# Optimization experiments

Measured on AMD Instinct MI355X. Metric: run time of the kernel, lower is better.

Reference implementation:

```python
import math
import jax, jax.numpy as jnp
import numpy as np

N = 2048          # batch size
D = 256           # embedding_dim
MEM = 16384       # memory_size
ANOMALY_WEIGHT = 1.0
TEMP = 0.1
MOMENTUM = 0.01
NCLS = 2          # binary phishing labels -> max(labels.max()+1, 2) == 2


def setup_inputs() -> dict:
    key = jax.random.key(0)
    ks = jax.random.split(key, 10)
    s = 1.0 / math.sqrt(D)  # nn.Linear default init range
    return {
        'z': jax.random.normal(ks[0], (N, D), jnp.float32),
        'labels': jax.random.randint(ks[1], (N,), 0, NCLS),
        'memory': jax.random.normal(ks[2], (MEM, D), jnp.float32),
        'memory_weights': jax.random.uniform(ks[3], (MEM,), jnp.float32),
        'running_mean': jnp.zeros((D,), jnp.float32),
        'running_cov': jnp.eye(D, dtype=jnp.float32),
        'Wq': jax.random.uniform(ks[4], (D, D), jnp.float32, -s, s),
        'bq': jax.random.uniform(ks[5], (D,), jnp.float32, -s, s),
        'Wk': jax.random.uniform(ks[6], (D, D), jnp.float32, -s, s),
        'bk': jax.random.uniform(ks[7], (D,), jnp.float32, -s, s),
        'Wv': jax.random.uniform(ks[8], (D, D), jnp.float32, -s, s),
        'bv': jax.random.uniform(ks[9], (D,), jnp.float32, -s, s),
    }


def reference(z, labels, memory, memory_weights, running_mean, running_cov,
              Wq, bq, Wk, bk, Wv, bv):
    # ---- update(z.detach(), labels): entire update path is detached in torch ----
    z_sg = jax.lax.stop_gradient(z)

    # _update_stats: EMA of batch mean / covariance (done before importance)
    mu = z_sg.mean(axis=0)                                  # [D]
    zc = z_sg - mu
    cov = zc.T @ zc / max(N - 1, 1)                         # [D, D]
    rm = (1.0 - MOMENTUM) * running_mean + MOMENTUM * mu
    rc = (1.0 - MOMENTUM) * running_cov + MOMENTUM * cov

    # _mahalanobis with updated running stats
    c = z_sg - rm
    cov_inv = jnp.linalg.inv(rc + 1e-6 * jnp.eye(D, dtype=rc.dtype))
    dist = jnp.sqrt(jnp.clip(jnp.einsum('nd,de,ne->n', c, cov_inv, c), 1e-8))
    a_norm = (dist - dist.min()) / (dist.max() - dist.min() + 1e-8)

    # _mi_proxy: KL(batch label dist || uniform), broadcast to all items
    counts = jnp.zeros((NCLS,), z.dtype).at[labels].add(1.0)
    p = counts / jnp.clip(counts.sum(), 1.0)
    # p / uniform == p * NCLS; clip inside log for safety (both classes present)
    kl = jnp.clip((p * jnp.log(jnp.clip(p * NCLS, 1e-8))).sum(), 0.0)
    importance = (1.0 + ANOMALY_WEIGHT * a_norm) * kl       # [N]

    # serial top-1 priority-queue eviction, in descending-importance order
    order = jnp.argsort(-importance)
    z_ord = z_sg[order]
    imp_ord = importance[order]

    def evict_step(state, inp):
        mem, w = state
        zi, imp = inp
        j = jnp.argmin(w)                   # weakest memory slot
        rep = imp > w[j]
        mem = mem.at[j].set(jnp.where(rep, zi, mem[j]))
        w = w.at[j].set(jnp.where(rep, imp, w[j]))
        return (mem, w), None

    (mem, _), _ = jax.lax.scan(evict_step, (memory, memory_weights), (z_ord, imp_ord))

    # ---- query(z): cross-attention over the (full) updated memory ----
    Q = z @ Wq.T + bq                       # [N, D]
    K = mem @ Wk.T + bk                     # [MEM, D]
    V = mem @ Wv.T + bv                     # [MEM, D]
    sc = (Q @ K.T) / math.sqrt(D)           # [N, MEM]
    attn = jax.nn.softmax(sc / TEMP, axis=-1)
    return z + 0.5 * (attn @ V)
```

## Files before the change

kernel.cpp:

```cpp
#include <hip/hip_runtime.h>
#include <math.h>

#define NB   2048
#define DE   256
#define MEMN 16384
#define CAND_CAP 256
#define FSPL 16
#define FKPS 1024
#define FIT  32

typedef __attribute__((ext_vector_type(8)))  short  short8;
typedef __attribute__((ext_vector_type(16))) float  float16;

static const size_t OFF_QB   = 0;
static const size_t OFF_KB   = 262144;
static const size_t OFF_VTB  = 2359296;
static const size_t OFF_LP   = 4456448;
static const size_t OFF_OPB  = 4521984;
static const size_t SO_A    = 0;
static const size_t SO_X    = 65536;
static const size_t SO_MUP  = 131072;
static const size_t SO_DIST = 147456;

__device__ inline unsigned short f2bf(float f) {
  unsigned u = __float_as_uint(f);
  unsigned r = (u + 0x7fffu + ((u >> 16) & 1u)) >> 16;
  return (unsigned short)r;
}
__device__ inline float bf2f(unsigned short s) {
  return __uint_as_float((unsigned)s << 16);
}

__device__ inline void bitonic_sort_u64(unsigned long long* key, int n, int tid, int nth) {
  for (int k = 2; k <= n; k <<= 1) {
    for (int j = k >> 1; j > 0; j >>= 1) {
      __syncthreads();
      for (int i = tid; i < n; i += nth) {
        int ixj = i ^ j;
        if (ixj > i) {
          unsigned long long a = key[i], b = key[ixj];
          bool up = ((i & k) == 0);
          if ((a > b) == up) { key[i] = b; key[ixj] = a; }
        }
      }
    }
  }
  __syncthreads();
}

__global__ __launch_bounds__(256) void mupart_kernel(const float* __restrict__ z,
                                                     float* __restrict__ mup,
                                                     float* __restrict__ Az) {
  int d = threadIdx.x;
  int r0 = blockIdx.x * 32;
  float4 zero4 = {0.f, 0.f, 0.f, 0.f};
  *(float4*)&Az[(size_t)blockIdx.x * 1024 + threadIdx.x * 4] = zero4;
  float s = 0.f;
  for (int r = 0; r < 32; ++r) s += z[(size_t)(r0 + r) * DE + d];
  mup[blockIdx.x * DE + d] = s;
}

__global__ __launch_bounds__(256) void covpart_kernel(const float* __restrict__ z,
                                                      float* __restrict__ A) {
  __shared__ float As[16][68];
  __shared__ float Bs[16][68];
  int tid = threadIdx.x, tx = tid & 15, ty = tid >> 4;
  int i0 = blockIdx.x * 64, j0 = blockIdx.y * 64;
  int nbase = blockIdx.z * 128;
  float acc[4][4] = {};
  for (int nt = 0; nt < 8; ++nt) {
    int n0 = nbase + nt * 16;
    for (int e = tid; e < 1024; e += 256) {
      int c = e & 63, nn = e >> 6;
      As[nn][c] = z[(size_t)(n0 + nn) * DE + i0 + c];
      Bs[nn][c] = z[(size_t)(n0 + nn) * DE + j0 + c];
    }
    __syncthreads();
#pragma unroll
    for (int nn = 0; nn < 16; ++nn) {
      float4 a4 = *(const float4*)&As[nn][ty * 4];
      float4 b4 = *(const float4*)&Bs[nn][tx * 4];
      acc[0][0] += a4.x*b4.x; acc[0][1] += a4.x*b4.y; acc[0][2] += a4.x*b4.z; acc[0][3] += a4.x*b4.w;
      acc[1][0] += a4.y*b4.x; acc[1][1] += a4.y*b4.y; acc[1][2] += a4.y*b4.z; acc[1][3] += a4.y*b4.w;
      acc[2][0] += a4.z*b4.x; acc[2][1] += a4.z*b4.y; acc[2][2] += a4.z*b4.z; acc[2][3] += a4.z*b4.w;
      acc[3][0] += a4.w*b4.x; acc[3][1] += a4.w*b4.y; acc[3][2] += a4.w*b4.z; acc[3][3] += a4.w*b4.w;
    }
    __syncthreads();
  }
  for (int r = 0; r < 4; ++r) {
    int i = i0 + ty * 4 + r;
    for (int c = 0; c < 4; ++c) {
      int j = j0 + tx * 4 + c;
      atomicAdd(&A[(size_t)i * DE + j], acc[r][c]);
    }
  }
}

__global__ __launch_bounds__(256) void gemmx_kernel(const float* __restrict__ ZtZ,
                                                    const float* __restrict__ rcov,
                                                    const float* __restrict__ mup,
                                                    float* __restrict__ X) {
  __shared__ float Ea[16][17];
  __shared__ float Eb[16][17];
  __shared__ float mus[256];
  int t = threadIdx.x, tx = t & 15, ty = t >> 4;
  int i0 = blockIdx.x * 16, j0 = blockIdx.y * 16;
  {
    float s = 0.f;
    for (int b = 0; b < 64; ++b) s += mup[b * DE + t];
    mus[t] = s;
  }
  __syncthreads();
  const float c1 = 0.01f / (float)(NB - 1);
  const float invN = 1.0f / (float)NB;
  float acc = 0.f;
  for (int k0 = 0; k0 < 256; k0 += 16) {
    int c = k0 + tx;
    {
      int r = i0 + ty;
      float base = 0.99f * rcov[(size_t)r * DE + c] +
                   c1 * (ZtZ[(size_t)r * DE + c] - mus[r] * mus[c] * invN);
      float e = -base;
      if (r == c) e += 1.0f - 1e-6f;
      Ea[ty][tx] = e;
    }
    {
      int r = j0 + ty;
      float base = 0.99f * rcov[(size_t)r * DE + c] +
                   c1 * (ZtZ[(size_t)r * DE + c] - mus[r] * mus[c] * invN);
      float e = -base;
      if (r == c) e += 1.0f - 1e-6f;
      Eb[ty][tx] = e;
    }
    __syncthreads();
#pragma unroll
    for (int k = 0; k < 16; ++k) acc += Ea[ty][k] * Eb[tx][k];
    __syncthreads();
  }
  int r = i0 + ty, c = j0 + tx;
  float base = 0.99f * rcov[(size_t)r * DE + c] +
               c1 * (ZtZ[(size_t)r * DE + c] - mus[r] * mus[c] * invN);
  float e = -base;
  if (r == c) e += 1.0f - 1e-6f;
  X[(size_t)r * DE + c] = acc + e + ((r == c) ? 1.0f : 0.0f);
}

__global__ __launch_bounds__(256) void dist_kernel(const float* __restrict__ z,
                                                   const float* __restrict__ rmean,
                                                   const float* __restrict__ mup,
                                                   const float* __restrict__ X,
                                                   float* __restrict__ dist) {
  __shared__ float cc[4][256];
  __shared__ float4 red[256];
  int n0 = blockIdx.x * 4, i = threadIdx.x;
  float s = 0.f;
  for (int b = 0; b < 64; ++b) s += mup[b * DE + i];
  float rmi = 0.99f * rmean[i] + 0.01f * s * (1.0f / (float)NB);
#pragma unroll
  for (int r = 0; r < 4; ++r) cc[r][i] = z[(size_t)(n0 + r) * DE + i] - rmi;
  __syncthreads();
  float y0 = 0.f, y1 = 0.f, y2 = 0.f, y3 = 0.f;
#pragma unroll 8
  for (int j = 0; j < DE; ++j) {
    float x = X[(size_t)j * DE + i];
    y0 += x * cc[0][j]; y1 += x * cc[1][j]; y2 += x * cc[2][j]; y3 += x * cc[3][j];
  }
  float4 v;
  v.x = y0 * cc[0][i]; v.y = y1 * cc[1][i]; v.z = y2 * cc[2][i]; v.w = y3 * cc[3][i];
  red[i] = v;
  __syncthreads();
  for (int sH = 128; sH > 0; sH >>= 1) {
    if (i < sH) {
      float4 a = red[i], b = red[i + sH];
      a.x += b.x; a.y += b.y; a.z += b.z; a.w += b.w;
      red[i] = a;
    }
    __syncthreads();
  }
  if (i < 4) {
    float4 tt = red[0];
    float d = (i == 0) ? tt.x : (i == 1) ? tt.y : (i == 2) ? tt.z : tt.w;
    dist[n0 + i] = sqrtf(fmaxf(d, 1e-8f));
  }
}

__global__ __launch_bounds__(1024) void update_kernel(const float* __restrict__ dist,
                                                      const int* __restrict__ labels,
                                                      const float* __restrict__ weights,
                                                      const float* __restrict__ z,
                                                      float* __restrict__ memory) {
  __shared__ unsigned long long ikeys[NB];
  __shared__ unsigned long long ck[CAND_CAP];
  __shared__ unsigned long long mred[1024];
  __shared__ int slots[CAND_CAP], srcs[CAND_CAP];
  __shared__ float smin[1024], smax[1024];
  __shared__ int scnt[1024];
  __shared__ float s_kl, s_dmin, s_inv;
  __shared__ int s_ccnt, s_m, s_stop;
  int t = threadIdx.x;

  float mn = 1e30f, mx = -1e30f; int c1 = 0;
  for (int n = t; n < NB; n += 1024) {
    float d = dist[n];
    mn = fminf(mn, d); mx = fmaxf(mx, d);
    c1 += labels[n];
  }
  smin[t] = mn; smax[t] = mx; scnt[t] = c1;
  __syncthreads();
  for (int s = 512; s > 0; s >>= 1) {
    if (t < s) {
      smin[t] = fminf(smin[t], smin[t + s]);
      smax[t] = fmaxf(smax[t], smax[t + s]);
      scnt[t] += scnt[t + s];
    }
    __syncthreads();
  }
  if (t == 0) {
    float p1 = (float)scnt[0] / (float)NB;
    float p0 = (float)(NB - scnt[0]) / (float)NB;
    float kl = p0 * logf(fmaxf(2.f * p0, 1e-8f)) + p1 * logf(fmaxf(2.f * p1, 1e-8f));
    s_kl = fmaxf(kl, 0.f);
    s_dmin = smin[0];
    s_inv = 1.0f / (smax[0] - smin[0] + 1e-8f);
    s_ccnt = 0; s_m = 0; s_stop = 0;
  }
  __syncthreads();
  float kl = s_kl;

  for (int n = t; n < NB; n += 1024) {
    float imp = (1.0f + (dist[n] - s_dmin) * s_inv) * kl;
    ikeys[n] = ((unsigned long long)(unsigned)(~__float_as_uint(imp)) << 32) | (unsigned)n;
  }
  float thresh = 2.f * kl;
  for (int j = t; j < MEMN; j += 1024) {
    float wv = weights[j];
    if (wv < thresh) {
      int p = atomicAdd(&s_ccnt, 1);
      if (p < CAND_CAP) ck[p] = ((unsigned long long)__float_as_uint(wv) << 32) | (unsigned)j;
    }
  }
  __syncthreads();
  int C = s_ccnt; if (C > CAND_CAP) C = CAND_CAP;
  for (int i = t; i < CAND_CAP; i += 1024)
    if (i >= C) ck[i] = 0xFFFFFFFFFFFFFFFFULL;
  bitonic_sort_u64(ck, CAND_CAP, t, 1024);

  float prevv = 0.f;
  for (int i = 0; i < C; ++i) {
    unsigned long long mymin = ikeys[t] < ikeys[t + 1024] ? ikeys[t] : ikeys[t + 1024];
    mred[t] = mymin;
    __syncthreads();
    for (int s = 512; s > 0; s >>= 1) {
      if (t < s) { if (mred[t + s] < mred[t]) mred[t] = mred[t + s]; }
      __syncthreads();
    }
    if (t == 0) {
      unsigned long long best = mred[0];
      float im = __uint_as_float(~(unsigned)(best >> 32));
      float wv = __uint_as_float((unsigned)(ck[i] >> 32));
      bool ok = (im > wv) && (i == 0 || prevv >= wv);
      if (ok) {
        slots[s_m] = (int)(ck[i] & 0xffffffffULL);
        srcs[s_m]  = (int)(best & 0xffffffffULL);
        s_m++;
        prevv = im;
        ikeys[(int)(best & 0xffffffffULL)] = ~0ULL;
      } else {
        s_stop = 1;
      }
    }
    __syncthreads();
    if (s_stop) break;
  }
  int m = s_m;
  for (int e = t; e < m * DE; e += 1024) {
    int i = e >> 8, d = e & 255;
    memory[(size_t)slots[i] * DE + d] = z[(size_t)srcs[i] * DE + d];
  }
}

__global__ __launch_bounds__(256, 1) void qkv_kernel(
    const float* __restrict__ z, const float* __restrict__ memory,
    const float* __restrict__ Wq, const float* __restrict__ bq,
    const float* __restrict__ Wk, const float* __restrict__ bk,
    const float* __restrict__ Wv, const float* __restrict__ bv,
    unsigned short* __restrict__ Qbf, unsigned short* __restrict__ Kbf,
    unsigned short* __restrict__ Vtb) {
  __shared__ unsigned short Bsh[64 * 264];
  int flat = blockIdx.x;
  const float *Af, *Bf, *bias;
  unsigned short* C;
  int bias_row, vtile, gx, gy, ldC;
  if (flat < 64) {
    gx = flat & 15; gy = flat >> 4;
    Af = z; Bf = Wq; bias = bq; bias_row = 0; vtile = 0; C = Qbf; ldC = DE;
  } else if (flat < 576) {
    int f = flat - 64; gx = f & 127; gy = f >> 7;
    Af = memory; Bf = Wk; bias = bk; bias_row = 0; vtile = 0; C = Kbf; ldC = DE;
  } else {
    int f = flat - 576; gx = f & 1; gy = f >> 1;
    Af = Wv; Bf = memory; bias = bv; bias_row = 1; vtile = 1; C = Vtb; ldC = 0;
  }

  int tid = threadIdx.x;
  int w = tid >> 6, lane = tid & 63;
  int m = lane & 31, h = lane >> 5;
  int arow = gx * 128 + w * 32 + m;
  int n0 = gy * 64;

  short8 af[16];
#pragma unroll
  for (int kc = 0; kc < 16; ++kc) {
    const float* src = &Af[(size_t)arow * DE + kc * 16 + h * 8];
    float4 f0 = *(const float4*)&src[0];
    float4 f1 = *(const float4*)&src[4];
    short8 v;
    v[0] = (short)f2bf(f0.x); v[1] = (short)f2bf(f0.y);
    v[2] = (short)f2bf(f0.z); v[3] = (short)f2bf(f0.w);
    v[4] = (short)f2bf(f1.x); v[5] = (short)f2bf(f1.y);
    v[6] = (short)f2bf(f1.z); v[7] = (short)f2bf(f1.w);
    af[kc] = v;
  }
  {
    int r = tid >> 2, q = tid & 3;
    const float* src = &Bf[(size_t)(n0 + r) * DE + q * 64];
    unsigned short* dst = &Bsh[r * 264 + q * 64];
#pragma unroll
    for (int j = 0; j < 8; ++j) {
      float4 f0 = *(const float4*)&src[j * 8];
      float4 f1 = *(const float4*)&src[j * 8 + 4];
      short8 v;
      v[0] = (short)f2bf(f0.x); v[1] = (short)f2bf(f0.y);
      v[2] = (short)f2bf(f0.z); v[3] = (short)f2bf(f0.w);
      v[4] = (short)f2bf(f1.x); v[5] = (short)f2bf(f1.y);
      v[6] = (short)f2bf(f1.z); v[7] = (short)f2bf(f1.w);
      *(short8*)&dst[j * 8] = v;
    }
  }
  __syncthreads();

  float16 a0 = {}, a1 = {};
#pragma unroll
  for (int kc = 0; kc < 16; ++kc) {
    short8 b0 = *(const short8*)&Bsh[(0 * 32 + m) * 264 + kc * 16 + h * 8];
    short8 b1 = *(const short8*)&Bsh[(1 * 32 + m) * 264 + kc * 16 + h * 8];
    a0 = __builtin_amdgcn_mfma_f32_32x32x16_bf16(af[kc], b0, a0, 0, 0, 0);
    a1 = __builtin_amdgcn_mfma_f32_32x32x16_bf16(af[kc], b1, a1, 0, 0, 0);
  }
#pragma unroll
  for (int r = 0; r < 16; ++r) {
    int rr = (r & 3) + 8 * (r >> 2) + 4 * h;
    int orow = gx * 128 + w * 32 + rr;
    int oc0 = n0 + m, oc1 = n0 + 32 + m;
    float bb0 = bias_row ? bias[orow] : bias[oc0];
    float bb1 = bias_row ? bias[orow] : bias[oc1];
    if (!vtile) {
      C[(size_t)orow * ldC + oc0] = f2bf(a0[r] + bb0);
      C[(size_t)orow * ldC + oc1] = f2bf(a1[r] + bb1);
    } else {
      C[(size_t)(oc0 >> 5) * 8192 + (size_t)orow * 32 + (oc0 & 31)] = f2bf(a0[r] + bb0);
      C[(size_t)(oc1 >> 5) * 8192 + (size_t)orow * 32 + (oc1 & 31)] = f2bf(a1[r] + bb1);
    }
  }
}

__global__ __launch_bounds__(256, 2) void flash_kernel(
    const unsigned short* __restrict__ Qb, const unsigned short* __restrict__ Kb,
    const unsigned short* __restrict__ Vtb, unsigned short* __restrict__ Opb,
    float* __restrict__ Lp) {
  __shared__ unsigned short Ks[32 * 264];
  __shared__ unsigned short Vs[128 * 40];
  __shared__ unsigned short Ps[4][32 * 40];

  int tid = threadIdx.x;
  int w = tid >> 6, lane = tid & 63;
  int m = lane & 31, h = lane >> 5;
  int sp = blockIdx.x, qg = blockIdx.y, dh = blockIdx.z;
  int myrow = qg * 128 + w * 32 + m;

  short8 qf[16];
#pragma unroll
  for (int kc = 0; kc < 16; ++kc)
    qf[kc] = *(const short8*)&Qb[(size_t)myrow * DE + kc * 16 + h * 8];
  short8 ones;
#pragma unroll
  for (int j = 0; j < 8; ++j) ones[j] = (short)0x3F80;

  float16 O[4] = {};
  float16 l = {};

  short8 kreg[4], vreg[2];
  {
    int kb = sp * FKPS;
#pragma unroll
    for (int i = 0; i < 4; ++i) {
      int c = i * 256 + tid, kr = c >> 5, kc = c & 31;
      kreg[i] = *(const short8*)&Kb[(size_t)(kb + kr) * DE + kc * 8];
    }
    const unsigned short* vg = &Vtb[(size_t)(kb >> 5) * 8192 + (size_t)dh * 4096];
#pragma unroll
    for (int i = 0; i < 2; ++i) {
      int c = i * 256 + tid;
      vreg[i] = *(const short8*)&vg[c * 8];
    }
  }

  for (int it = 0; it < FIT; ++it) {
    __syncthreads();
#pragma unroll
    for (int i = 0; i < 4; ++i) {
      int c = i * 256 + tid, kr = c >> 5, kc = c & 31;
      *(short8*)&Ks[kr * 264 + kc * 8] = kreg[i];
    }
#pragma unroll
    for (int i = 0; i < 2; ++i) {
      int c = i * 256 + tid, dr = c >> 2, dc = c & 3;
      *(short8*)&Vs[dr * 40 + dc * 8] = vreg[i];
    }
    if (it + 1 < FIT) {
      int kb = sp * FKPS + (it + 1) * 32;
#pragma unroll
      for (int i = 0; i < 4; ++i) {
        int c = i * 256 + tid, kr = c >> 5, kc = c & 31;
        kreg[i] = *(const short8*)&Kb[(size_t)(kb + kr) * DE + kc * 8];
      }
      const unsigned short* vg = &Vtb[(size_t)(kb >> 5) * 8192 + (size_t)dh * 4096];
#pragma unroll
      for (int i = 0; i < 2; ++i) {
        int c = i * 256 + tid;
        vreg[i] = *(const short8*)&vg[c * 8];
      }
    }
    __syncthreads();

    float16 s0 = {}, s1 = {};
#pragma unroll
    for (int kc = 0; kc < 16; kc += 2) {
      short8 b0 = *(const short8*)&Ks[m * 264 + kc * 16 + h * 8];
      short8 b1 = *(const short8*)&Ks[m * 264 + (kc + 1) * 16 + h * 8];
      s0 = __builtin_amdgcn_mfma_f32_32x32x16_bf16(qf[kc], b0, s0, 0, 0, 0);
      s1 = __builtin_amdgcn_mfma_f32_32x32x16_bf16(qf[kc + 1], b1, s1, 0, 0, 0);
    }
#pragma unroll
    for (int r = 0; r < 16; ++r) {
      int row = (r & 3) + 8 * (r >> 2) + 4 * h;
      Ps[w][row * 40 + m] = f2bf(__expf(fmaf(s0[r] + s1[r], 0.625f, -11.0903549f)));
    }
    short8 pa0 = *(const short8*)&Ps[w][m * 40 + h * 8];
    short8 pa1 = *(const short8*)&Ps[w][m * 40 + 16 + h * 8];
    l = __builtin_amdgcn_mfma_f32_32x32x16_bf16(pa0, ones, l, 0, 0, 0);
    l = __builtin_amdgcn_mfma_f32_32x32x16_bf16(pa1, ones, l, 0, 0, 0);
#pragma unroll
    for (int ct = 0; ct < 4; ++ct) {
      short8 vb0 = *(const short8*)&Vs[(ct * 32 + m) * 40 + h * 8];
      short8 vb1 = *(const short8*)&Vs[(ct * 32 + m) * 40 + 16 + h * 8];
      O[ct] = __builtin_amdgcn_mfma_f32_32x32x16_bf16(pa0, vb0, O[ct], 0, 0, 0);
      O[ct] = __builtin_amdgcn_mfma_f32_32x32x16_bf16(pa1, vb1, O[ct], 0, 0, 0);
    }
  }

  size_t ob = ((size_t)sp * NB + qg * 128 + w * 32) * DE + dh * 128;
#pragma unroll
  for (int ct = 0; ct < 4; ++ct)
#pragma unroll
    for (int r = 0; r < 16; ++r) {
      int rr = (r & 3) + 8 * (r >> 2) + 4 * h;
      Opb[ob + (size_t)rr * DE + ct * 32 + m] = f2bf(O[ct][r]);
    }
  if (dh == 0 && m == 0) {
#pragma unroll
    for (int r = 0; r < 16; ++r) {
      int rr = (r & 3) + 8 * (r >> 2) + 4 * h;
      Lp[sp * NB + qg * 128 + w * 32 + rr] = l[r];
    }
  }
}

__global__ __launch_bounds__(256) void combine_kernel(const float* __restrict__ z,
                                                      const unsigned short* __restrict__ Opb,
                                                      const float* __restrict__ Lp,
                                                      float* __restrict__ out) {
  int n = blockIdx.x, c = threadIdx.x;
  float num = 0.f, den = 0.f;
#pragma unroll
  for (int s = 0; s < FSPL; ++s) {
    den += Lp[s * NB + n];
    num += bf2f(Opb[((size_t)s * NB + n) * DE + c]);
  }
  size_t base = (size_t)n * DE + c;
  out[base] = z[base] + 0.5f * num / den;
}

extern "C" void kernel_launch(void* const* d_in, const int* in_sizes, int n_in,
                              void* d_out, int out_size, void* d_ws, size_t ws_size,
                              hipStream_t stream) {
  (void)in_sizes; (void)n_in; (void)out_size; (void)ws_size;
  const float* z       = (const float*)d_in[0];
  const int*   labels  = (const int*)d_in[1];
  float*       memory  = (float*)d_in[2];
  const float* weights = (const float*)d_in[3];
  const float* rmean   = (const float*)d_in[4];
  const float* rcov    = (const float*)d_in[5];
  const float* Wq      = (const float*)d_in[6];
  const float* bq      = (const float*)d_in[7];
  const float* Wk      = (const float*)d_in[8];
  const float* bk      = (const float*)d_in[9];
  const float* Wv      = (const float*)d_in[10];
  const float* bv      = (const float*)d_in[11];
  float* out = (float*)d_out;
  float* ws  = (float*)d_ws;

  unsigned short* Qbf = (unsigned short*)(ws + OFF_QB);
  unsigned short* Kbf = (unsigned short*)(ws + OFF_KB);
  unsigned short* Vtb = (unsigned short*)(ws + OFF_VTB);
  float* Lp           = ws + OFF_LP;
  unsigned short* Opb = (unsigned short*)(ws + OFF_OPB);
  float* SB    = ws + OFF_OPB;
  float* A     = SB + SO_A;
  float* X     = SB + SO_X;
  float* mup   = SB + SO_MUP;
  float* dist  = SB + SO_DIST;

  mupart_kernel<<<64, 256, 0, stream>>>(z, mup, A);
  covpart_kernel<<<dim3(4, 4, 16), 256, 0, stream>>>(z, A);
  gemmx_kernel<<<dim3(16, 16), 256, 0, stream>>>(A, rcov, mup, X);
  dist_kernel<<<NB / 4, 256, 0, stream>>>(z, rmean, mup, X, dist);
  update_kernel<<<1, 1024, 0, stream>>>(dist, labels, weights, z, memory);
  qkv_kernel<<<1088, 256, 0, stream>>>(z, memory, Wq, bq, Wk, bk, Wv, bv, Qbf, Kbf, Vtb);
  flash_kernel<<<dim3(FSPL, NB / 128, 2), 256, 0, stream>>>(Qbf, Kbf, Vtb, Opb, Lp);
  combine_kernel<<<NB, 256, 0, stream>>>(z, Opb, Lp, out);
}
```

Before: 260.1 us.

## Use uneven 24-way key split in flash attention and fold mean into covariance kernel

The flash attention key range is split into 24 uneven chunks (8 of 768 keys, 16 of 640) when the workspace is large enough, instead of 16 equal chunks. This gives more blocks to fill the GPU's compute units. The separate mean-partial kernel is removed: diagonal covariance blocks compute column sums, and a memset zeroes the accumulator. The combine kernel loops over a runtime split count. The extra partial outputs need more workspace, which is why the 24-way path is gated on ws_size.

```diff
diff --git a/kernel.cpp b/kernel.cpp
--- a/kernel.cpp
+++ b/kernel.cpp
@@ -5,9 +5,6 @@
 #define DE   256
 #define MEMN 16384
 #define CAND_CAP 256
-#define FSPL 16
-#define FKPS 1024
-#define FIT  32
 
 typedef __attribute__((ext_vector_type(8)))  short  short8;
 typedef __attribute__((ext_vector_type(16))) float  float16;
@@ -17,10 +14,11 @@
 static const size_t OFF_VTB  = 2359296;
 static const size_t OFF_LP   = 4456448;
 static const size_t OFF_OPB  = 4521984;
+static const size_t END24    = 10813440;
 static const size_t SO_A    = 0;
 static const size_t SO_X    = 65536;
 static const size_t SO_MUP  = 131072;
-static const size_t SO_DIST = 147456;
+static const size_t SO_DIST = 135168;
 
 __device__ inline unsigned short f2bf(float f) {
   unsigned u = __float_as_uint(f);
@@ -48,20 +46,9 @@
   __syncthreads();
 }
 
-__global__ __launch_bounds__(256) void mupart_kernel(const float* __restrict__ z,
-                                                     float* __restrict__ mup,
-                                                     float* __restrict__ Az) {
-  int d = threadIdx.x;
-  int r0 = blockIdx.x * 32;
-  float4 zero4 = {0.f, 0.f, 0.f, 0.f};
-  *(float4*)&Az[(size_t)blockIdx.x * 1024 + threadIdx.x * 4] = zero4;
-  float s = 0.f;
-  for (int r = 0; r < 32; ++r) s += z[(size_t)(r0 + r) * DE + d];
-  mup[blockIdx.x * DE + d] = s;
-}
-
 __global__ __launch_bounds__(256) void covpart_kernel(const float* __restrict__ z,
-                                                      float* __restrict__ A) {
+                                                      float* __restrict__ A,
+                                                      float* __restrict__ mup) {
   __shared__ float As[16][68];
   __shared__ float Bs[16][68];
   int tid = threadIdx.x, tx = tid & 15, ty = tid >> 4;
@@ -94,6 +81,12 @@
       atomicAdd(&A[(size_t)i * DE + j], acc[r][c]);
     }
   }
+  if (blockIdx.x == blockIdx.y && tid < 64) {
+    int col = i0 + tid;
+    float s = 0.f;
+    for (int r = 0; r < 128; ++r) s += z[(size_t)(nbase + r) * DE + col];
+    mup[blockIdx.z * DE + col] = s;
+  }
 }
 
 __global__ __launch_bounds__(256) void gemmx_kernel(const float* __restrict__ ZtZ,
@@ -107,7 +100,8 @@
   int i0 = blockIdx.x * 16, j0 = blockIdx.y * 16;
   {
     float s = 0.f;
-    for (int b = 0; b < 64; ++b) s += mup[b * DE + t];
+#pragma unroll
+    for (int b = 0; b < 16; ++b) s += mup[b * DE + t];
     mus[t] = s;
   }
   __syncthreads();
@@ -154,7 +148,8 @@
   __shared__ float4 red[256];
   int n0 = blockIdx.x * 4, i = threadIdx.x;
   float s = 0.f;
-  for (int b = 0; b < 64; ++b) s += mup[b * DE + i];
+#pragma unroll
+  for (int b = 0; b < 16; ++b) s += mup[b * DE + i];
   float rmi = 0.99f * rmean[i] + 0.01f * s * (1.0f / (float)NB);
 #pragma unroll
   for (int r = 0; r < 4; ++r) cc[r][i] = z[(size_t)(n0 + r) * DE + i] - rmi;
@@ -367,7 +362,7 @@
 __global__ __launch_bounds__(256, 2) void flash_kernel(
     const unsigned short* __restrict__ Qb, const unsigned short* __restrict__ Kb,
     const unsigned short* __restrict__ Vtb, unsigned short* __restrict__ Opb,
-    float* __restrict__ Lp) {
+    float* __restrict__ Lp, int spl) {
   __shared__ unsigned short Ks[32 * 264];
   __shared__ unsigned short Vs[128 * 40];
   __shared__ unsigned short Ps[4][32 * 40];
@@ -378,6 +373,14 @@
   int sp = blockIdx.x, qg = blockIdx.y, dh = blockIdx.z;
   int myrow = qg * 128 + w * 32 + m;
 
+  int kb0, fit;
+  if (spl == 24) {
+    if (sp < 8) { kb0 = sp * 768; fit = 24; }
+    else        { kb0 = 6144 + (sp - 8) * 640; fit = 20; }
+  } else {
+    kb0 = sp * 1024; fit = 32;
+  }
+
   short8 qf[16];
 #pragma unroll
   for (int kc = 0; kc < 16; ++kc)
@@ -391,7 +394,7 @@
 
   short8 kreg[4], vreg[2];
   {
-    int kb = sp * FKPS;
+    int kb = kb0;
 #pragma unroll
     for (int i = 0; i < 4; ++i) {
       int c = i * 256 + tid, kr = c >> 5, kc = c & 31;
@@ -405,7 +408,7 @@
     }
   }
 
-  for (int it = 0; it < FIT; ++it) {
+  for (int it = 0; it < fit; ++it) {
     __syncthreads();
 #pragma unroll
     for (int i = 0; i < 4; ++i) {
@@ -417,8 +420,8 @@
       int c = i * 256 + tid, dr = c >> 2, dc = c & 3;
       *(short8*)&Vs[dr * 40 + dc * 8] = vreg[i];
     }
-    if (it + 1 < FIT) {
-      int kb = sp * FKPS + (it + 1) * 32;
+    if (it + 1 < fit) {
+      int kb = kb0 + (it + 1) * 32;
 #pragma unroll
       for (int i = 0; i < 4; ++i) {
         int c = i * 256 + tid, kr = c >> 5, kc = c & 31;
@@ -479,11 +482,10 @@
 __global__ __launch_bounds__(256) void combine_kernel(const float* __restrict__ z,
                                                       const unsigned short* __restrict__ Opb,
                                                       const float* __restrict__ Lp,
-                                                      float* __restrict__ out) {
+                                                      float* __restrict__ out, int spl) {
   int n = blockIdx.x, c = threadIdx.x;
   float num = 0.f, den = 0.f;
-#pragma unroll
-  for (int s = 0; s < FSPL; ++s) {
+  for (int s = 0; s < spl; ++s) {
     den += Lp[s * NB + n];
     num += bf2f(Opb[((size_t)s * NB + n) * DE + c]);
   }
@@ -494,7 +496,7 @@
 extern "C" void kernel_launch(void* const* d_in, const int* in_sizes, int n_in,
                               void* d_out, int out_size, void* d_ws, size_t ws_size,
                               hipStream_t stream) {
-  (void)in_sizes; (void)n_in; (void)out_size; (void)ws_size;
+  (void)in_sizes; (void)n_in; (void)out_size;
   const float* z       = (const float*)d_in[0];
   const int*   labels  = (const int*)d_in[1];
   float*       memory  = (float*)d_in[2];
@@ -521,12 +523,14 @@
   float* mup   = SB + SO_MUP;
   float* dist  = SB + SO_DIST;
 
-  mupart_kernel<<<64, 256, 0, stream>>>(z, mup, A);
-  covpart_kernel<<<dim3(4, 4, 16), 256, 0, stream>>>(z, A);
+  int spl = (ws_size >= END24 * sizeof(float)) ? 24 : 16;
+
+  hipMemsetAsync(A, 0, 65536 * sizeof(float), stream);
+  covpart_kernel<<<dim3(4, 4, 16), 256, 0, stream>>>(z, A, mup);
   gemmx_kernel<<<dim3(16, 16), 256, 0, stream>>>(A, rcov, mup, X);
   dist_kernel<<<NB / 4, 256, 0, stream>>>(z, rmean, mup, X, dist);
   update_kernel<<<1, 1024, 0, stream>>>(dist, labels, weights, z, memory);
   qkv_kernel<<<1088, 256, 0, stream>>>(z, memory, Wq, bq, Wk, bk, Wv, bv, Qbf, Kbf, Vtb);
-  flash_kernel<<<dim3(FSPL, NB / 128, 2), 256, 0, stream>>>(Qbf, Kbf, Vtb, Opb, Lp);
-  combine_kernel<<<NB, 256, 0, stream>>>(z, Opb, Lp, out);
-}
+  flash_kernel<<<dim3(spl, NB / 128, 2), 256, 0, stream>>>(Qbf, Kbf, Vtb, Opb, Lp, spl);
+  combine_kernel<<<NB, 256, 0, stream>>>(z, Opb, Lp, out, spl);
+}
```

Result: slower. 272.1 us (+4.6%).
